# Kernel optimization log

Measured on AMD Instinct MI355X. Metric: run time of the kernel, lower is better.

The kernel has to match this reference:

```python
import jax, jax.numpy as jnp
import numpy as np

N_NODES = 100000
N_EDGES = 1600000
IN_C, HID_C, OUT_C = 128, 128, 64


def gcn_conv(x, src, dst, n_nodes, W, b):
    # PyG GCNConv (normalize=True, add_self_loops=True):
    # out = D^{-1/2} (A+I) D^{-1/2} (x @ W^T) + b
    h = x @ W.T                                   # [N, out]
    deg = jax.ops.segment_sum(jnp.ones(src.shape, x.dtype), dst,
                              num_segments=n_nodes)  # includes self-loops
    dinv = jnp.where(deg > 0, jax.lax.rsqrt(deg), 0.0)
    norm = dinv[src] * dinv[dst]                  # [E+N]
    msg = h[src] * norm[:, None]                  # gather + scale
    out = jax.ops.segment_sum(msg, dst, num_segments=n_nodes)
    return out + b


def setup_inputs() -> dict:
    key = jax.random.key(0)
    ks = jax.random.split(key, 8)
    x = jax.random.normal(ks[0], (N_NODES, IN_C), dtype=jnp.float32)
    edge_index = jax.random.randint(ks[1], (2, N_EDGES), 0, N_NODES, dtype=jnp.int64)

    def lin(k, fan_out, fan_in):
        s = 1.0 / np.sqrt(fan_in)
        kw, kb = jax.random.split(k)
        W = jax.random.uniform(kw, (fan_out, fan_in), jnp.float32, -s, s)
        b = jax.random.uniform(kb, (fan_out,), jnp.float32, -s, s)
        return W, b

    W1, b1 = lin(ks[2], HID_C, IN_C)
    W2, b2 = lin(ks[3], HID_C, HID_C)
    W3, b3 = lin(ks[4], OUT_C, HID_C)
    return {"x": x, "edge_index": edge_index,
            "W1": W1, "b1": b1, "W2": W2, "b2": b2, "W3": W3, "b3": b3}


def reference(x, edge_index, W1, b1, W2, b2, W3, b3):
    n = x.shape[0]
    loop = jnp.arange(n, dtype=edge_index.dtype)
    src = jnp.concatenate([edge_index[0], loop])  # add self-loops once; identical per layer
    dst = jnp.concatenate([edge_index[1], loop])
    h = gcn_conv(x, src, dst, n, W1, b1)
    h = jax.nn.relu(h)
    h = gcn_conv(h, src, dst, n, W2, b2)
    h = jax.nn.relu(h)
    h = gcn_conv(h, src, dst, n, W3, b3)
    return h
```

## Files before the change

kernel.cpp:

```cpp
#include <hip/hip_runtime.h>


#define NPB 256
#define CAP 4672
#define BIN_WGS 128

typedef short bfrag __attribute__((ext_vector_type(8)));
typedef float f32x4 __attribute__((ext_vector_type(4)));
typedef unsigned short u16x8 __attribute__((ext_vector_type(8)));

__global__ __launch_bounds__(256) void init_cur(int* __restrict__ cur, int B) {
  int i = blockIdx.x * 256 + threadIdx.x;
  if (i < B) cur[i] = i * CAP;
}

__global__ __launch_bounds__(256) void bin_edges(const int* __restrict__ src,
                                                 const int* __restrict__ dst,
                                                 int* __restrict__ cur,
                                                 int* __restrict__ binned,
                                                 int E, int B) {
  __shared__ int lc[512];
  __shared__ int lbase[512];
  const int t = threadIdx.x;
  const int chunk = (E + BIN_WGS - 1) / BIN_WGS;
  const int e0 = blockIdx.x * chunk;
  const int e1 = min(E, e0 + chunk);

  for (int i = t; i < B; i += 256) lc[i] = 0;
  __syncthreads();
  for (int e = e0 + t; e < e1; e += 256) {
    int d = dst[e];
    atomicAdd(&lc[d >> 8], 1);
  }
  __syncthreads();
  for (int i = t; i < B; i += 256) {
    int c = lc[i];
    lbase[i] = c ? atomicAdd(&cur[i], c) : 0;
    lc[i] = 0;
  }
  __syncthreads();
  for (int e = e0 + t; e < e1; e += 256) {
    int d = dst[e];
    int s = __builtin_nontemporal_load(&src[e]);
    int bk = d >> 8;
    int p = lbase[bk] + atomicAdd(&lc[bk], 1);
    if (p < (bk + 1) * CAP)
      binned[p] = ((d & 255) << 24) | s;
  }
}

__global__ __launch_bounds__(256) void build_buckets(const int* __restrict__ binned,
                                                     const int* __restrict__ cur,
                                                     int* __restrict__ cols,
                                                     int2* __restrict__ off2,
                                                     float* __restrict__ dinv,
                                                     int N) {
  __shared__ int eb[CAP];
  __shared__ int ob[CAP];
  __shared__ int lc[256];
  __shared__ int sc[256];
  const int b = blockIdx.x;
  const int t = threadIdx.x;
  const int base = b * CAP;
  const int cntb = min(cur[b] - base, CAP);

  for (int i = t; i < cntb; i += 256) eb[i] = binned[base + i];
  lc[t] = 0;
  __syncthreads();
  for (int i = t; i < cntb; i += 256)
    atomicAdd(&lc[(unsigned)eb[i] >> 24], 1);
  __syncthreads();
  int myc = lc[t];
  sc[t] = myc;
  __syncthreads();
  for (int d = 1; d < 256; d <<= 1) {
    int a = (t >= d) ? sc[t - d] : 0;
    __syncthreads();
    sc[t] += a;
    __syncthreads();
  }
  int excl = sc[t] - myc;
  int node = b * NPB + t;
  if (node < N) {
    off2[node] = make_int2(base + excl, base + excl + myc);
    dinv[node] = rsqrtf((float)(myc + 1));
  }
  lc[t] = excl;
  __syncthreads();
  for (int i = t; i < cntb; i += 256) {
    int e = eb[i];
    int p = atomicAdd(&lc[(unsigned)e >> 24], 1);
    ob[p] = e & 0xFFFFFF;
  }
  __syncthreads();
  for (int i = t; i < cntb; i += 256) cols[base + i] = ob[i];
}

__device__ inline unsigned short bf16rne(float x) {
  unsigned u = __float_as_uint(x);
  return (unsigned short)((u + 0x7FFFu + ((u >> 16) & 1u)) >> 16);
}
__device__ inline float bf16lo(unsigned q) { return __uint_as_float(q << 16); }
__device__ inline float bf16hi(unsigned q) { return __uint_as_float(q & 0xFFFF0000u); }

__global__ __launch_bounds__(256) void split_w(const float* __restrict__ W,
                                               unsigned short* __restrict__ hi,
                                               unsigned short* __restrict__ lo,
                                               int total) {
  int i = blockIdx.x * 256 + threadIdx.x;
  if (i < total) {
    float v = W[i];
    unsigned short h = bf16rne(v);
    hi[i] = h;
    lo[i] = bf16rne(v - __uint_as_float((unsigned)h << 16));
  }
}

#define LDP 136
template <int OUTC>
__global__ __launch_bounds__(256) void gemm_xw_mfma(const float* __restrict__ X,
                                                    const unsigned short* __restrict__ Whg,
                                                    const unsigned short* __restrict__ Wlg,
                                                    const float* __restrict__ dinv,
                                                    unsigned short* __restrict__ Y,
                                                    int M) {
  __shared__ unsigned short Xhi[64 * LDP], Xlo[64 * LDP];
  __shared__ unsigned short Whi[64 * LDP], Wlo[64 * LDP];
  const int tid = threadIdx.x;
  const int m_base = blockIdx.x * 64;

  for (int idx = tid; idx < 64 * 16; idx += 256) {
    int r = idx >> 4, g = idx & 15;
    int m = m_base + r;
    float4 v0 = make_float4(0.f, 0.f, 0.f, 0.f), v1 = v0;
    if (m < M) {
      const float4* px = (const float4*)(X + (size_t)m * 128 + g * 8);
      v0 = px[0];
      v1 = px[1];
    }
    float vv[8] = {v0.x, v0.y, v0.z, v0.w, v1.x, v1.y, v1.z, v1.w};
    u16x8 hv, lv;
#pragma unroll
    for (int j = 0; j < 8; ++j) {
      unsigned short h = bf16rne(vv[j]);
      float res = vv[j] - __uint_as_float((unsigned)h << 16);
      hv[j] = h;
      lv[j] = bf16rne(res);
    }
    *(u16x8*)(Xhi + r * LDP + g * 8) = hv;
    *(u16x8*)(Xlo + r * LDP + g * 8) = lv;
  }

  const int lane = tid & 63;
  const int wv = tid >> 6;
  const int col_l = lane & 15;
  const int quad = lane >> 4;
  const int aBase = (wv * 16 + col_l) * LDP + quad * 8;
  const int bBase = col_l * LDP + quad * 8;

  for (int cc = 0; cc < OUTC; cc += 64) {
    __syncthreads();
    for (int idx = tid; idx < 64 * 16; idx += 256) {
      int r = idx >> 4, g = idx & 15;
      u16x8 hv = *(const u16x8*)(Whg + (size_t)(cc + r) * 128 + g * 8);
      u16x8 lv = *(const u16x8*)(Wlg + (size_t)(cc + r) * 128 + g * 8);
      *(u16x8*)(Whi + r * LDP + g * 8) = hv;
      *(u16x8*)(Wlo + r * LDP + g * 8) = lv;
    }
    __syncthreads();

    f32x4 acc[4] = {{0.f, 0.f, 0.f, 0.f},
                    {0.f, 0.f, 0.f, 0.f},
                    {0.f, 0.f, 0.f, 0.f},
                    {0.f, 0.f, 0.f, 0.f}};
#pragma unroll
    for (int ks = 0; ks < 4; ++ks) {
      int ao = aBase + ks * 32;
      bfrag aHi = *(const bfrag*)(Xhi + ao);
      bfrag aLo = *(const bfrag*)(Xlo + ao);
#pragma unroll
      for (int t = 0; t < 4; ++t) {
        int bo = bBase + t * 16 * LDP + ks * 32;
        bfrag bHi = *(const bfrag*)(Whi + bo);
        bfrag bLo = *(const bfrag*)(Wlo + bo);
        acc[t] = __builtin_amdgcn_mfma_f32_16x16x32_bf16(aHi, bHi, acc[t], 0, 0, 0);
        acc[t] = __builtin_amdgcn_mfma_f32_16x16x32_bf16(aLo, bHi, acc[t], 0, 0, 0);
        acc[t] = __builtin_amdgcn_mfma_f32_16x16x32_bf16(aHi, bLo, acc[t], 0, 0, 0);
      }
    }

#pragma unroll
    for (int r = 0; r < 4; ++r) {
      int row = m_base + wv * 16 + quad * 4 + r;
      if (row < M) {
        float s = dinv[row];
#pragma unroll
        for (int t = 0; t < 4; ++t) {
          unsigned short h = bf16rne(acc[t][r] * s);
          Y[(size_t)row * OUTC + cc + t * 16 + col_l] = h;
        }
      }
    }
  }
}

template <int C, bool RELU>
__global__ __launch_bounds__(256) void aggregate2(const unsigned short* __restrict__ xs,
                                                  const int2* __restrict__ off2,
                                                  const int* __restrict__ cols,
                                                  const float* __restrict__ dinv,
                                                  const float* __restrict__ bias,
                                                  float* __restrict__ out, int N) {
  constexpr int CG = C / 8;
  constexpr int EG = 64 / CG;
  int wid = (int)((blockIdx.x * blockDim.x + threadIdx.x) >> 6);
  int lane = threadIdx.x & 63;
  if (wid >= N) return;
  const int eg = lane / CG;
  const int cg = lane % CG;

  float acc[8] = {0.f, 0.f, 0.f, 0.f, 0.f, 0.f, 0.f, 0.f};
  if (eg == 0) {
    uint4 d = *(const uint4*)(xs + (size_t)wid * C + cg * 8);
    acc[0] = bf16lo(d.x); acc[1] = bf16hi(d.x);
    acc[2] = bf16lo(d.y); acc[3] = bf16hi(d.y);
    acc[4] = bf16lo(d.z); acc[5] = bf16hi(d.z);
    acc[6] = bf16lo(d.w); acc[7] = bf16hi(d.w);
  }

  int2 oo = off2[wid];
  int ebase = oo.x;
  const int eend = oo.y;
  while (ebase < eend) {
    int cnt = eend - ebase;
    if (cnt > 64) cnt = 64;
    int col = (lane < cnt) ? __builtin_nontemporal_load(&cols[ebase + lane]) : 0;
    const int c1 = cnt - 1;
    for (int j = 0; j < cnt; j += 4 * EG) {
      int i0 = j + eg, i1 = i0 + EG, i2 = i1 + EG, i3 = i2 + EG;
      int s0 = __shfl(col, min(i0, c1));
      int s1 = __shfl(col, min(i1, c1));
      int s2 = __shfl(col, min(i2, c1));
      int s3 = __shfl(col, min(i3, c1));
      uint4 d0 = *(const uint4*)(xs + (size_t)s0 * C + cg * 8);
      uint4 d1 = *(const uint4*)(xs + (size_t)s1 * C + cg * 8);
      uint4 d2 = *(const uint4*)(xs + (size_t)s2 * C + cg * 8);
      uint4 d3 = *(const uint4*)(xs + (size_t)s3 * C + cg * 8);
      if (i0 < cnt) {
        acc[0] += bf16lo(d0.x); acc[1] += bf16hi(d0.x);
        acc[2] += bf16lo(d0.y); acc[3] += bf16hi(d0.y);
        acc[4] += bf16lo(d0.z); acc[5] += bf16hi(d0.z);
        acc[6] += bf16lo(d0.w); acc[7] += bf16hi(d0.w);
      }
      if (i1 < cnt) {
        acc[0] += bf16lo(d1.x); acc[1] += bf16hi(d1.x);
        acc[2] += bf16lo(d1.y); acc[3] += bf16hi(d1.y);
        acc[4] += bf16lo(d1.z); acc[5] += bf16hi(d1.z);
        acc[6] += bf16lo(d1.w); acc[7] += bf16hi(d1.w);
      }
      if (i2 < cnt) {
        acc[0] += bf16lo(d2.x); acc[1] += bf16hi(d2.x);
        acc[2] += bf16lo(d2.y); acc[3] += bf16hi(d2.y);
        acc[4] += bf16lo(d2.z); acc[5] += bf16hi(d2.z);
        acc[6] += bf16lo(d2.w); acc[7] += bf16hi(d2.w);
      }
      if (i3 < cnt) {
        acc[0] += bf16lo(d3.x); acc[1] += bf16hi(d3.x);
        acc[2] += bf16lo(d3.y); acc[3] += bf16hi(d3.y);
        acc[4] += bf16lo(d3.z); acc[5] += bf16hi(d3.z);
        acc[6] += bf16lo(d3.w); acc[7] += bf16hi(d3.w);
      }
    }
    ebase += cnt;
  }

#pragma unroll
  for (int m = CG; m < 64; m <<= 1) {
#pragma unroll
    for (int q = 0; q < 8; ++q) acc[q] += __shfl_xor(acc[q], m);
  }

  if (eg == 0) {
    float dd = dinv[wid];
    const float4 bA = *(const float4*)(bias + cg * 8);
    const float4 bB = *(const float4*)(bias + cg * 8 + 4);
    f32x4 oA, oB;
    oA[0] = acc[0] * dd + bA.x; oA[1] = acc[1] * dd + bA.y;
    oA[2] = acc[2] * dd + bA.z; oA[3] = acc[3] * dd + bA.w;
    oB[0] = acc[4] * dd + bB.x; oB[1] = acc[5] * dd + bB.y;
    oB[2] = acc[6] * dd + bB.z; oB[3] = acc[7] * dd + bB.w;
    if (RELU) {
#pragma unroll
      for (int q = 0; q < 4; ++q) {
        oA[q] = fmaxf(oA[q], 0.f);
        oB[q] = fmaxf(oB[q], 0.f);
      }
    }
    __builtin_nontemporal_store(oA, (f32x4*)(out + (size_t)wid * C + cg * 8));
    __builtin_nontemporal_store(oB, (f32x4*)(out + (size_t)wid * C + cg * 8 + 4));
  }
}


extern "C" void kernel_launch(void* const* d_in, const int* in_sizes, int n_in,
                              void* d_out, int out_size, void* d_ws, size_t ws_size,
                              hipStream_t stream) {
  const float* x  = (const float*)d_in[0];
  const int*   ei = (const int*)d_in[1];
  const float* W1 = (const float*)d_in[2];
  const float* b1 = (const float*)d_in[3];
  const float* W2 = (const float*)d_in[4];
  const float* b2 = (const float*)d_in[5];
  const float* W3 = (const float*)d_in[6];
  const float* b3 = (const float*)d_in[7];

  const int N = in_sizes[0] / 128;
  const int E = in_sizes[1] / 2;
  const int* src = ei;
  const int* dst = ei + E;
  const int B = (N + NPB - 1) / NPB;

  char* w = (char*)d_ws;
  size_t p = 0;
  auto alloc = [&](size_t bytes) -> void* {
    void* r = w + p;
    p = (p + bytes + 255) & ~(size_t)255;
    return r;
  };
  float*    dinv   = (float*)alloc((size_t)N * 4);
  int2*     off2   = (int2*)alloc((size_t)N * 8);
  int*      cur    = (int*)alloc((size_t)B * 4);
  int*      binned = (int*)alloc((size_t)B * CAP * 4);
  int*      cols   = (int*)alloc((size_t)B * CAP * 4);
  unsigned short* xsb = (unsigned short*)alloc((size_t)N * 128 * 2);
  float*    bufB   = (float*)alloc((size_t)N * 128 * 4);
  unsigned short* w1h = (unsigned short*)alloc(128 * 128 * 2);
  unsigned short* w1l = (unsigned short*)alloc(128 * 128 * 2);
  unsigned short* w2h = (unsigned short*)alloc(128 * 128 * 2);
  unsigned short* w2l = (unsigned short*)alloc(128 * 128 * 2);
  unsigned short* w3h = (unsigned short*)alloc(64 * 128 * 2);
  unsigned short* w3l = (unsigned short*)alloc(64 * 128 * 2);

  init_cur<<<(B + 255) / 256, 256, 0, stream>>>(cur, B);
  bin_edges<<<BIN_WGS, 256, 0, stream>>>(src, dst, cur, binned, E, B);
  split_w<<<64, 256, 0, stream>>>(W1, w1h, w1l, 128 * 128);
  split_w<<<64, 256, 0, stream>>>(W2, w2h, w2l, 128 * 128);
  split_w<<<32, 256, 0, stream>>>(W3, w3h, w3l, 64 * 128);
  build_buckets<<<B, 256, 0, stream>>>(binned, cur, cols, off2, dinv, N);

  const int gb = (N + 63) / 64;
  const int ab = (N + 3) / 4;

  gemm_xw_mfma<128><<<gb, 256, 0, stream>>>(x, w1h, w1l, dinv, xsb, N);
  aggregate2<128, true><<<ab, 256, 0, stream>>>(xsb, off2, cols, dinv, b1, bufB, N);
  gemm_xw_mfma<128><<<gb, 256, 0, stream>>>(bufB, w2h, w2l, dinv, xsb, N);
  aggregate2<128, true><<<ab, 256, 0, stream>>>(xsb, off2, cols, dinv, b2, bufB, N);
  gemm_xw_mfma<64><<<gb, 256, 0, stream>>>(bufB, w3h, w3l, dinv, xsb, N);
  aggregate2<64, false><<<ab, 256, 0, stream>>>(xsb, off2, cols, dinv, b3,
                                                (float*)d_out, N);
}
```

Baseline: 443.6 us.

## Fuse aggregation with next layer's GEMM and raise binning workgroup count

Adds an agg_gemm kernel that aggregates neighbor rows for a 64-node tile, applies bias and ReLU, splits the result into bf16 hi/lo in shared memory, and immediately multiplies by the next layer's weights with MFMA. This removes the fp32 intermediate buffer write and its re-read between layers 1-2 and 2-3. Each wave now handles 16 rows sequentially with 4 edge groups, which changes gather parallelism and may lower occupancy because of the larger shared memory use. BIN_WGS is also raised from 128 to 512 so edge binning is spread across more workgroups.

```diff
diff --git a/kernel.cpp b/kernel.cpp
--- a/kernel.cpp
+++ b/kernel.cpp
@@ -3,7 +3,7 @@
 
 #define NPB 256
 #define CAP 4672
-#define BIN_WGS 128
+#define BIN_WGS 512
 
 typedef short bfrag __attribute__((ext_vector_type(8)));
 typedef float f32x4 __attribute__((ext_vector_type(4)));
@@ -197,6 +197,165 @@
 #pragma unroll
         for (int t = 0; t < 4; ++t) {
           unsigned short h = bf16rne(acc[t][r] * s);
+          Y[(size_t)row * OUTC + cc + t * 16 + col_l] = h;
+        }
+      }
+    }
+  }
+}
+
+template <int OUTC, bool RELU>
+__global__ __launch_bounds__(256) void agg_gemm(const unsigned short* __restrict__ xs,
+                                                const int2* __restrict__ off2,
+                                                const int* __restrict__ cols,
+                                                const float* __restrict__ dinv,
+                                                const float* __restrict__ bias,
+                                                const unsigned short* __restrict__ Whg,
+                                                const unsigned short* __restrict__ Wlg,
+                                                unsigned short* __restrict__ Y,
+                                                int N) {
+  __shared__ unsigned short Xhi[64 * LDP], Xlo[64 * LDP];
+  __shared__ unsigned short Whi[64 * LDP], Wlo[64 * LDP];
+  const int tid = threadIdx.x;
+  const int lane = tid & 63;
+  const int wv = tid >> 6;
+  const int eg = lane >> 4;
+  const int cg = lane & 15;
+  const int m_base = blockIdx.x * 64;
+
+  for (int r = 0; r < 16; ++r) {
+    const int row = wv * 16 + r;
+    const int wid = m_base + row;
+    float acc[8] = {0.f, 0.f, 0.f, 0.f, 0.f, 0.f, 0.f, 0.f};
+    if (wid < N) {
+      if (eg == 0) {
+        uint4 d = *(const uint4*)(xs + (size_t)wid * 128 + cg * 8);
+        acc[0] = bf16lo(d.x); acc[1] = bf16hi(d.x);
+        acc[2] = bf16lo(d.y); acc[3] = bf16hi(d.y);
+        acc[4] = bf16lo(d.z); acc[5] = bf16hi(d.z);
+        acc[6] = bf16lo(d.w); acc[7] = bf16hi(d.w);
+      }
+      int2 oo = off2[wid];
+      int ebase = oo.x;
+      const int eend = oo.y;
+      while (ebase < eend) {
+        int cnt = eend - ebase;
+        if (cnt > 64) cnt = 64;
+        int col = (lane < cnt) ? __builtin_nontemporal_load(&cols[ebase + lane]) : 0;
+        const int c1 = cnt - 1;
+        for (int j = 0; j < cnt; j += 16) {
+          int i0 = j + eg, i1 = i0 + 4, i2 = i1 + 4, i3 = i2 + 4;
+          int s0 = __shfl(col, min(i0, c1));
+          int s1 = __shfl(col, min(i1, c1));
+          int s2 = __shfl(col, min(i2, c1));
+          int s3 = __shfl(col, min(i3, c1));
+          uint4 d0 = *(const uint4*)(xs + (size_t)s0 * 128 + cg * 8);
+          uint4 d1 = *(const uint4*)(xs + (size_t)s1 * 128 + cg * 8);
+          uint4 d2 = *(const uint4*)(xs + (size_t)s2 * 128 + cg * 8);
+          uint4 d3 = *(const uint4*)(xs + (size_t)s3 * 128 + cg * 8);
+          if (i0 < cnt) {
+            acc[0] += bf16lo(d0.x); acc[1] += bf16hi(d0.x);
+            acc[2] += bf16lo(d0.y); acc[3] += bf16hi(d0.y);
+            acc[4] += bf16lo(d0.z); acc[5] += bf16hi(d0.z);
+            acc[6] += bf16lo(d0.w); acc[7] += bf16hi(d0.w);
+          }
+          if (i1 < cnt) {
+            acc[0] += bf16lo(d1.x); acc[1] += bf16hi(d1.x);
+            acc[2] += bf16lo(d1.y); acc[3] += bf16hi(d1.y);
+            acc[4] += bf16lo(d1.z); acc[5] += bf16hi(d1.z);
+            acc[6] += bf16lo(d1.w); acc[7] += bf16hi(d1.w);
+          }
+          if (i2 < cnt) {
+            acc[0] += bf16lo(d2.x); acc[1] += bf16hi(d2.x);
+            acc[2] += bf16lo(d2.y); acc[3] += bf16hi(d2.y);
+            acc[4] += bf16lo(d2.z); acc[5] += bf16hi(d2.z);
+            acc[6] += bf16lo(d2.w); acc[7] += bf16hi(d2.w);
+          }
+          if (i3 < cnt) {
+            acc[0] += bf16lo(d3.x); acc[1] += bf16hi(d3.x);
+            acc[2] += bf16lo(d3.y); acc[3] += bf16hi(d3.y);
+            acc[4] += bf16lo(d3.z); acc[5] += bf16hi(d3.z);
+            acc[6] += bf16lo(d3.w); acc[7] += bf16hi(d3.w);
+          }
+        }
+        ebase += cnt;
+      }
+#pragma unroll
+      for (int m = 16; m < 64; m <<= 1) {
+#pragma unroll
+        for (int q = 0; q < 8; ++q) acc[q] += __shfl_xor(acc[q], m);
+      }
+      if (eg == 0) {
+        float dd = dinv[wid];
+        const float4 bA = *(const float4*)(bias + cg * 8);
+        const float4 bB = *(const float4*)(bias + cg * 8 + 4);
+        float h[8];
+        h[0] = acc[0] * dd + bA.x; h[1] = acc[1] * dd + bA.y;
+        h[2] = acc[2] * dd + bA.z; h[3] = acc[3] * dd + bA.w;
+        h[4] = acc[4] * dd + bB.x; h[5] = acc[5] * dd + bB.y;
+        h[6] = acc[6] * dd + bB.z; h[7] = acc[7] * dd + bB.w;
+        u16x8 hv, lv;
+#pragma unroll
+        for (int q = 0; q < 8; ++q) {
+          float v = RELU ? fmaxf(h[q], 0.f) : h[q];
+          unsigned short hb = bf16rne(v);
+          hv[q] = hb;
+          lv[q] = bf16rne(v - __uint_as_float((unsigned)hb << 16));
+        }
+        *(u16x8*)(Xhi + row * LDP + cg * 8) = hv;
+        *(u16x8*)(Xlo + row * LDP + cg * 8) = lv;
+      }
+    } else if (eg == 0) {
+      u16x8 z = {0, 0, 0, 0, 0, 0, 0, 0};
+      *(u16x8*)(Xhi + row * LDP + cg * 8) = z;
+      *(u16x8*)(Xlo + row * LDP + cg * 8) = z;
+    }
+  }
+
+  const int col_l = cg;
+  const int quad = eg;
+  const int aBase = (wv * 16 + col_l) * LDP + quad * 8;
+  const int bBase = col_l * LDP + quad * 8;
+
+  for (int cc = 0; cc < OUTC; cc += 64) {
+    __syncthreads();
+    for (int idx = tid; idx < 64 * 16; idx += 256) {
+      int r = idx >> 4, g = idx & 15;
+      u16x8 hv = *(const u16x8*)(Whg + (size_t)(cc + r) * 128 + g * 8);
+      u16x8 lv = *(const u16x8*)(Wlg + (size_t)(cc + r) * 128 + g * 8);
+      *(u16x8*)(Whi + r * LDP + g * 8) = hv;
+      *(u16x8*)(Wlo + r * LDP + g * 8) = lv;
+    }
+    __syncthreads();
+
+    f32x4 acc4[4] = {{0.f, 0.f, 0.f, 0.f},
+                     {0.f, 0.f, 0.f, 0.f},
+                     {0.f, 0.f, 0.f, 0.f},
+                     {0.f, 0.f, 0.f, 0.f}};
+#pragma unroll
+    for (int ks = 0; ks < 4; ++ks) {
+      int ao = aBase + ks * 32;
+      bfrag aHi = *(const bfrag*)(Xhi + ao);
+      bfrag aLo = *(const bfrag*)(Xlo + ao);
+#pragma unroll
+      for (int t = 0; t < 4; ++t) {
+        int bo = bBase + t * 16 * LDP + ks * 32;
+        bfrag bHi = *(const bfrag*)(Whi + bo);
+        bfrag bLo = *(const bfrag*)(Wlo + bo);
+        acc4[t] = __builtin_amdgcn_mfma_f32_16x16x32_bf16(aHi, bHi, acc4[t], 0, 0, 0);
+        acc4[t] = __builtin_amdgcn_mfma_f32_16x16x32_bf16(aLo, bHi, acc4[t], 0, 0, 0);
+        acc4[t] = __builtin_amdgcn_mfma_f32_16x16x32_bf16(aHi, bLo, acc4[t], 0, 0, 0);
+      }
+    }
+
+#pragma unroll
+    for (int r = 0; r < 4; ++r) {
+      int row = m_base + wv * 16 + quad * 4 + r;
+      if (row < N) {
+        float s = dinv[row];
+#pragma unroll
+        for (int t = 0; t < 4; ++t) {
+          unsigned short h = bf16rne(acc4[t][r] * s);
           Y[(size_t)row * OUTC + cc + t * 16 + col_l] = h;
         }
       }
@@ -332,8 +491,9 @@
   int*      cur    = (int*)alloc((size_t)B * 4);
   int*      binned = (int*)alloc((size_t)B * CAP * 4);
   int*      cols   = (int*)alloc((size_t)B * CAP * 4);
-  unsigned short* xsb = (unsigned short*)alloc((size_t)N * 128 * 2);
-  float*    bufB   = (float*)alloc((size_t)N * 128 * 4);
+  unsigned short* xs1 = (unsigned short*)alloc((size_t)N * 128 * 2);
+  unsigned short* xs2 = (unsigned short*)alloc((size_t)N * 128 * 2);
+  unsigned short* xs3 = (unsigned short*)alloc((size_t)N * 64 * 2);
   unsigned short* w1h = (unsigned short*)alloc(128 * 128 * 2);
   unsigned short* w1l = (unsigned short*)alloc(128 * 128 * 2);
   unsigned short* w2h = (unsigned short*)alloc(128 * 128 * 2);
@@ -351,11 +511,11 @@
   const int gb = (N + 63) / 64;
   const int ab = (N + 3) / 4;
 
-  gemm_xw_mfma<128><<<gb, 256, 0, stream>>>(x, w1h, w1l, dinv, xsb, N);
-  aggregate2<128, true><<<ab, 256, 0, stream>>>(xsb, off2, cols, dinv, b1, bufB, N);
-  gemm_xw_mfma<128><<<gb, 256, 0, stream>>>(bufB, w2h, w2l, dinv, xsb, N);
-  aggregate2<128, true><<<ab, 256, 0, stream>>>(xsb, off2, cols, dinv, b2, bufB, N);
-  gemm_xw_mfma<64><<<gb, 256, 0, stream>>>(bufB, w3h, w3l, dinv, xsb, N);
-  aggregate2<64, false><<<ab, 256, 0, stream>>>(xsb, off2, cols, dinv, b3,
+  gemm_xw_mfma<128><<<gb, 256, 0, stream>>>(x, w1h, w1l, dinv, xs1, N);
+  agg_gemm<128, true><<<gb, 256, 0, stream>>>(xs1, off2, cols, dinv, b1,
+                                              w2h, w2l, xs2, N);
+  agg_gemm<64, true><<<gb, 256, 0, stream>>>(xs2, off2, cols, dinv, b2,
+                                             w3h, w3l, xs3, N);
+  aggregate2<64, false><<<ab, 256, 0, stream>>>(xs3, off2, cols, dinv, b3,
                                                 (float*)d_out, N);
 }
```

Result: slower. 591.6 us (+33.4%).
